# Performance work log

Hardware: AMD Instinct MI355X
Metric: run time of the kernel (lower is better)

## Reference

```python
import jax, jax.numpy as jnp
import numpy as np

N_NODES = 100000


def _gcn_conv(x, W, b, src, dst, ew, num_nodes):
    # PyG GCNConv: symmetric normalization with self-loops already included
    # in (src, dst, ew). deg computed on destination (col) index.
    deg = jax.ops.segment_sum(ew, dst, num_segments=num_nodes)  # [N]
    dinv = jnp.where(deg > 0, jax.lax.rsqrt(deg), 0.0)          # [N]
    norm = dinv[src] * ew * dinv[dst]                           # [E]
    h = x @ W                                                   # [N, out]
    msg = h[src] * norm[:, None]                                # [E, out] gather+scale
    out = jax.ops.segment_sum(msg, dst, num_segments=num_nodes) # scatter-add
    return out + b


def setup_inputs() -> dict:
    key = jax.random.key(0)
    k = jax.random.split(key, 8)
    in_c, hid_c, out_c = 128, 128, 64
    E, EL = 1600000, 200000
    x = jax.random.normal(k[0], (N_NODES, in_c), dtype=jnp.float32)
    edge_index = jax.random.randint(k[1], (2, E), 0, N_NODES, dtype=jnp.int64)
    edge_weight = jax.random.uniform(k[2], (E,), dtype=jnp.float32)
    edge_label_index = jax.random.randint(k[3], (2, EL), 0, N_NODES, dtype=jnp.int64)
    # Glorot-ish params
    W1 = jax.random.normal(k[4], (in_c, hid_c), dtype=jnp.float32) / np.sqrt(in_c)
    b1 = jnp.zeros((hid_c,), dtype=jnp.float32)
    W2 = jax.random.normal(k[5], (hid_c, out_c), dtype=jnp.float32) / np.sqrt(hid_c)
    b2 = jnp.zeros((out_c,), dtype=jnp.float32)
    return {"x": x, "edge_index": edge_index, "edge_weight": edge_weight,
            "edge_label_index": edge_label_index,
            "W1": W1, "b1": b1, "W2": W2, "b2": b2}


def reference(x, edge_index, edge_weight, edge_label_index, W1, b1, W2, b2):
    n = x.shape[0]
    # add self-loops (weight 1.0), static shape
    loop = jnp.arange(n, dtype=edge_index.dtype)
    src = jnp.concatenate([edge_index[0], loop])
    dst = jnp.concatenate([edge_index[1], loop])
    ew = jnp.concatenate([edge_weight, jnp.ones((n,), dtype=edge_weight.dtype)])
    h = jax.nn.relu(_gcn_conv(x, W1, b1, src, dst, ew, n))
    z = _gcn_conv(h, W2, b2, src, dst, ew, n)          # [N, out_c]
    # decode: edge dot-product
    return (z[edge_label_index[0]] * z[edge_label_index[1]]).sum(axis=-1)
```

## Files before the change

kernel.cpp:

```cpp
#include <hip/hip_runtime.h>
#include <math.h>

__global__ __launch_bounds__(256) void gemm128_hist_kernel(
        const float* __restrict__ X, const float* __restrict__ W, float* __restrict__ Y, int n,
        const int* __restrict__ dst, int* __restrict__ cnt, int* __restrict__ rank, int E) {
    constexpr int CG  = 32;
    constexpr int RG  = 8;
    constexpr int M   = 64;
    constexpr int RT  = 8;
    constexpr int KC  = 32;
    constexpr int LDX = 132;
    __shared__ float  Xl[M * LDX];
    __shared__ float4 Wl[KC * CG];

    const int bid = blockIdx.x;
    const int t = threadIdx.x;
    const int EPB = (E + (int)gridDim.x - 1) / (int)gridDim.x;
    const int eBeg = bid * EPB;
    const int eEnd = min(eBeg + EPB, E);

    if ((bid & 1) == 0) {
        for (int e = eBeg + t; e < eEnd; e += 256)
            rank[e] = atomicAdd(&cnt[dst[e]], 1);
    }

    int row0 = bid * M;
    {
        const float4* Xg = (const float4*)X;
        for (int f = t; f < M * 32; f += 256) {
            int r = f >> 5, c4 = f & 31;
            int gr = row0 + r;
            float4 v = make_float4(0.f, 0.f, 0.f, 0.f);
            if (gr < n) v = Xg[(size_t)gr * 32 + c4];
            *(float4*)&Xl[r * LDX + c4 * 4] = v;
        }
    }

    int cg = t % CG;
    int r0 = (t / CG) * RT;

    float4 acc[RT];
#pragma unroll
    for (int r = 0; r < RT; r++) acc[r] = make_float4(0.f, 0.f, 0.f, 0.f);

    const float4* Wg = (const float4*)W;
    for (int kc = 0; kc < 128; kc += KC) {
        __syncthreads();
        for (int f = t; f < KC * CG; f += 256)
            Wl[f] = Wg[(size_t)kc * CG + f];
        __syncthreads();
#pragma unroll 4
        for (int k = 0; k < KC; k += 4) {
            float4 b0 = Wl[(k + 0) * CG + cg];
            float4 b1 = Wl[(k + 1) * CG + cg];
            float4 b2 = Wl[(k + 2) * CG + cg];
            float4 b3 = Wl[(k + 3) * CG + cg];
#pragma unroll
            for (int r = 0; r < RT; r++) {
                float4 a = *(float4*)&Xl[(r0 + r) * LDX + kc + k];
                acc[r].x += a.x * b0.x + a.y * b1.x + a.z * b2.x + a.w * b3.x;
                acc[r].y += a.x * b0.y + a.y * b1.y + a.z * b2.y + a.w * b3.y;
                acc[r].z += a.x * b0.z + a.y * b1.z + a.z * b2.z + a.w * b3.z;
                acc[r].w += a.x * b0.w + a.y * b1.w + a.z * b2.w + a.w * b3.w;
            }
        }
    }

#pragma unroll
    for (int r = 0; r < RT; r++) {
        int gr = row0 + r0 + r;
        if (gr < n) *(float4*)&Y[(size_t)gr * 128 + cg * 4] = acc[r];
    }

    if (bid & 1) {
        for (int e = eBeg + t; e < eEnd; e += 256)
            rank[e] = atomicAdd(&cnt[dst[e]], 1);
    }
}

__global__ __launch_bounds__(256) void scan_block(const int* __restrict__ in, int* __restrict__ out,
                                                  int* __restrict__ bsum, int n) {
    __shared__ int s[256];
    int tid = threadIdx.x;
    int base = blockIdx.x * 1024 + tid * 4;
    int a0 = (base + 0 < n) ? in[base + 0] : 0;
    int a1 = (base + 1 < n) ? in[base + 1] : 0;
    int a2 = (base + 2 < n) ? in[base + 2] : 0;
    int a3 = (base + 3 < n) ? in[base + 3] : 0;
    int tsum = a0 + a1 + a2 + a3;
    s[tid] = tsum;
    __syncthreads();
    for (int off = 1; off < 256; off <<= 1) {
        int v = (tid >= off) ? s[tid - off] : 0;
        __syncthreads();
        s[tid] += v;
        __syncthreads();
    }
    int texcl = s[tid] - tsum;
    if (base + 0 < n) out[base + 0] = texcl;
    if (base + 1 < n) out[base + 1] = texcl + a0;
    if (base + 2 < n) out[base + 2] = texcl + a0 + a1;
    if (base + 3 < n) out[base + 3] = texcl + a0 + a1 + a2;
    if (tid == 255) bsum[blockIdx.x] = s[255];
}

__global__ __launch_bounds__(256) void scan_bsums(int* __restrict__ bsum, int nb) {
    __shared__ int s[256];
    __shared__ int carry_s;
    int tid = threadIdx.x;
    if (tid == 0) carry_s = 0;
    __syncthreads();
    for (int base = 0; base < nb; base += 256) {
        int v = (base + tid < nb) ? bsum[base + tid] : 0;
        int orig = v;
        s[tid] = v;
        __syncthreads();
        for (int off = 1; off < 256; off <<= 1) {
            int u = (tid >= off) ? s[tid - off] : 0;
            __syncthreads();
            s[tid] += u;
            __syncthreads();
        }
        int carry = carry_s;
        int excl = s[tid] - orig + carry;
        if (base + tid < nb) bsum[base + tid] = excl;
        int tot = s[255];
        __syncthreads();
        if (tid == 0) carry_s = carry + tot;
        __syncthreads();
    }
}

__global__ void scan_add(int* __restrict__ rowptr, const int* __restrict__ bscan, int n) {
    int t = blockIdx.x * blockDim.x + threadIdx.x;
    if (t < n) rowptr[t] += bscan[t >> 10];
}

__global__ void scatter_pairs(const int* __restrict__ src, const int* __restrict__ dst,
                              const float* __restrict__ ew, const int* __restrict__ rowptr,
                              const int* __restrict__ rank, int2* __restrict__ pairs, int E) {
    int e = blockIdx.x * blockDim.x + threadIdx.x;
    if (e >= E) return;
    int d = dst[e];
    int p = rowptr[d] + rank[e];
    pairs[p] = make_int2(src[e], __float_as_int(ew[e]));
}

__global__ void deg_dinv_kernel(const int2* __restrict__ pairs, const int* __restrict__ rowptr,
                                float* __restrict__ dinv, int n) {
    int i = blockIdx.x * blockDim.x + threadIdx.x;
    if (i >= n) return;
    int beg = rowptr[i], end = rowptr[i + 1];
    float s = 0.f;
    for (int j = beg; j < end; j++) s += __int_as_float(pairs[j].y);
    dinv[i] = 1.0f / sqrtf(s + 1.0f);
}

__global__ __launch_bounds__(256) void gather_mv_kernel(const float* __restrict__ H,
                                                        const int* __restrict__ rowptr,
                                                        const int2* __restrict__ pairs,
                                                        const float* __restrict__ dinv,
                                                        const float* __restrict__ bias,
                                                        const float* __restrict__ W2,
                                                        float* __restrict__ Z, int n) {
    __shared__ float h1s[8 * 128];
    __shared__ float w2s[128 * 64];
    const int t = threadIdx.x;
    const int nl = t >> 5;
    const int c4 = t & 31;
    const int node = blockIdx.x * 8 + nl;
    const float4* H4 = (const float4*)H;

    {
        const float4* W2g = (const float4*)W2;
        float4* w2s4 = (float4*)w2s;
#pragma unroll
        for (int f = 0; f < 8; f++) w2s4[f * 256 + t] = W2g[f * 256 + t];
    }

    float4 a0 = make_float4(0.f, 0.f, 0.f, 0.f);
    if (node < n) {
        int beg = rowptr[node], end = rowptr[node + 1];
        float di = dinv[node];
        float4 hv = H4[(size_t)node * 32 + c4];
        a0.x = hv.x * di; a0.y = hv.y * di; a0.z = hv.z * di; a0.w = hv.w * di;
        float4 a1 = make_float4(0.f, 0.f, 0.f, 0.f);
        float4 a2 = make_float4(0.f, 0.f, 0.f, 0.f);
        float4 a3 = make_float4(0.f, 0.f, 0.f, 0.f);
        int j = beg;
        for (; j + 8 <= end; j += 8) {
            int2 p0 = pairs[j + 0], p1 = pairs[j + 1], p2 = pairs[j + 2], p3 = pairs[j + 3];
            int2 p4 = pairs[j + 4], p5 = pairs[j + 5], p6 = pairs[j + 6], p7 = pairs[j + 7];
            float4 v0 = H4[(size_t)p0.x * 32 + c4];
            float4 v1 = H4[(size_t)p1.x * 32 + c4];
            float4 v2 = H4[(size_t)p2.x * 32 + c4];
            float4 v3 = H4[(size_t)p3.x * 32 + c4];
            float4 v4 = H4[(size_t)p4.x * 32 + c4];
            float4 v5 = H4[(size_t)p5.x * 32 + c4];
            float4 v6 = H4[(size_t)p6.x * 32 + c4];
            float4 v7 = H4[(size_t)p7.x * 32 + c4];
            float w0 = dinv[p0.x] * __int_as_float(p0.y);
            float w1 = dinv[p1.x] * __int_as_float(p1.y);
            float w2 = dinv[p2.x] * __int_as_float(p2.y);
            float w3 = dinv[p3.x] * __int_as_float(p3.y);
            float w4 = dinv[p4.x] * __int_as_float(p4.y);
            float w5 = dinv[p5.x] * __int_as_float(p5.y);
            float w6 = dinv[p6.x] * __int_as_float(p6.y);
            float w7 = dinv[p7.x] * __int_as_float(p7.y);
            a0.x += v0.x * w0; a0.y += v0.y * w0; a0.z += v0.z * w0; a0.w += v0.w * w0;
            a1.x += v1.x * w1; a1.y += v1.y * w1; a1.z += v1.z * w1; a1.w += v1.w * w1;
            a2.x += v2.x * w2; a2.y += v2.y * w2; a2.z += v2.z * w2; a2.w += v2.w * w2;
            a3.x += v3.x * w3; a3.y += v3.y * w3; a3.z += v3.z * w3; a3.w += v3.w * w3;
            a0.x += v4.x * w4; a0.y += v4.y * w4; a0.z += v4.z * w4; a0.w += v4.w * w4;
            a1.x += v5.x * w5; a1.y += v5.y * w5; a1.z += v5.z * w5; a1.w += v5.w * w5;
            a2.x += v6.x * w6; a2.y += v6.y * w6; a2.z += v6.z * w6; a2.w += v6.w * w6;
            a3.x += v7.x * w7; a3.y += v7.y * w7; a3.z += v7.z * w7; a3.w += v7.w * w7;
        }
        if (j + 4 <= end) {
            int2 p0 = pairs[j + 0], p1 = pairs[j + 1], p2 = pairs[j + 2], p3 = pairs[j + 3];
            float4 v0 = H4[(size_t)p0.x * 32 + c4];
            float4 v1 = H4[(size_t)p1.x * 32 + c4];
            float4 v2 = H4[(size_t)p2.x * 32 + c4];
            float4 v3 = H4[(size_t)p3.x * 32 + c4];
            float w0 = dinv[p0.x] * __int_as_float(p0.y);
            float w1 = dinv[p1.x] * __int_as_float(p1.y);
            float w2 = dinv[p2.x] * __int_as_float(p2.y);
            float w3 = dinv[p3.x] * __int_as_float(p3.y);
            a0.x += v0.x * w0; a0.y += v0.y * w0; a0.z += v0.z * w0; a0.w += v0.w * w0;
            a1.x += v1.x * w1; a1.y += v1.y * w1; a1.z += v1.z * w1; a1.w += v1.w * w1;
            a2.x += v2.x * w2; a2.y += v2.y * w2; a2.z += v2.z * w2; a2.w += v2.w * w2;
            a3.x += v3.x * w3; a3.y += v3.y * w3; a3.z += v3.z * w3; a3.w += v3.w * w3;
            j += 4;
        }
        for (; j < end; j++) {
            int2 pr = pairs[j];
            float w = dinv[pr.x] * __int_as_float(pr.y);
            float4 v = H4[(size_t)pr.x * 32 + c4];
            a0.x += v.x * w; a0.y += v.y * w; a0.z += v.z * w; a0.w += v.w * w;
        }
        float4 bb = ((const float4*)bias)[c4];
        a0.x = fmaxf(((a0.x + a1.x) + (a2.x + a3.x)) * di + bb.x, 0.f);
        a0.y = fmaxf(((a0.y + a1.y) + (a2.y + a3.y)) * di + bb.y, 0.f);
        a0.z = fmaxf(((a0.z + a1.z) + (a2.z + a3.z)) * di + bb.z, 0.f);
        a0.w = fmaxf(((a0.w + a1.w) + (a2.w + a3.w)) * di + bb.w, 0.f);
    }
    *(float4*)&h1s[nl * 128 + c4 * 4] = a0;
    __syncthreads();

    float z0 = 0.f, z1 = 0.f;
    const float* hrow = &h1s[nl * 128];
    const float2* w2c = (const float2*)w2s;
#pragma unroll 8
    for (int k = 0; k < 128; k++) {
        float hk = hrow[k];
        float2 w = w2c[k * 32 + c4];
        z0 += hk * w.x;
        z1 += hk * w.y;
    }
    if (node < n) *(float2*)&Z[(size_t)node * 64 + c4 * 2] = make_float2(z0, z1);
}

template<int C, bool RELU>
__global__ __launch_bounds__(256) void gather_reduce(const float* __restrict__ H,
                                                     const int* __restrict__ rowptr,
                                                     const int2* __restrict__ pairs,
                                                     const float* __restrict__ dinv,
                                                     const float* __restrict__ bias,
                                                     float* __restrict__ out, int n) {
    constexpr int TPN = C / 4;
    int t = blockIdx.x * blockDim.x + threadIdx.x;
    int node = t / TPN;
    int c4 = t % TPN;
    if (node >= n) return;
    const float4* H4 = (const float4*)H;
    int beg = rowptr[node], end = rowptr[node + 1];
    float di = dinv[node];
    float4 hv = H4[(size_t)node * TPN + c4];
    float4 bb = ((const float4*)bias)[c4];
    float4 a0, a1, a2, a3;
    a0.x = hv.x * di; a0.y = hv.y * di; a0.z = hv.z * di; a0.w = hv.w * di;
    a1 = make_float4(0.f, 0.f, 0.f, 0.f);
    a2 = make_float4(0.f, 0.f, 0.f, 0.f);
    a3 = make_float4(0.f, 0.f, 0.f, 0.f);
    int j = beg;
    for (; j + 8 <= end; j += 8) {
        int2 p0 = pairs[j + 0], p1 = pairs[j + 1], p2 = pairs[j + 2], p3 = pairs[j + 3];
        int2 p4 = pairs[j + 4], p5 = pairs[j + 5], p6 = pairs[j + 6], p7 = pairs[j + 7];
        float4 v0 = H4[(size_t)p0.x * TPN + c4];
        float4 v1 = H4[(size_t)p1.x * TPN + c4];
        float4 v2 = H4[(size_t)p2.x * TPN + c4];
        float4 v3 = H4[(size_t)p3.x * TPN + c4];
        float4 v4 = H4[(size_t)p4.x * TPN + c4];
        float4 v5 = H4[(size_t)p5.x * TPN + c4];
        float4 v6 = H4[(size_t)p6.x * TPN + c4];
        float4 v7 = H4[(size_t)p7.x * TPN + c4];
        float w0 = dinv[p0.x] * __int_as_float(p0.y);
        float w1 = dinv[p1.x] * __int_as_float(p1.y);
        float w2 = dinv[p2.x] * __int_as_float(p2.y);
        float w3 = dinv[p3.x] * __int_as_float(p3.y);
        float w4 = dinv[p4.x] * __int_as_float(p4.y);
        float w5 = dinv[p5.x] * __int_as_float(p5.y);
        float w6 = dinv[p6.x] * __int_as_float(p6.y);
        float w7 = dinv[p7.x] * __int_as_float(p7.y);
        a0.x += v0.x * w0; a0.y += v0.y * w0; a0.z += v0.z * w0; a0.w += v0.w * w0;
        a1.x += v1.x * w1; a1.y += v1.y * w1; a1.z += v1.z * w1; a1.w += v1.w * w1;
        a2.x += v2.x * w2; a2.y += v2.y * w2; a2.z += v2.z * w2; a2.w += v2.w * w2;
        a3.x += v3.x * w3; a3.y += v3.y * w3; a3.z += v3.z * w3; a3.w += v3.w * w3;
        a0.x += v4.x * w4; a0.y += v4.y * w4; a0.z += v4.z * w4; a0.w += v4.w * w4;
        a1.x += v5.x * w5; a1.y += v5.y * w5; a1.z += v5.z * w5; a1.w += v5.w * w5;
        a2.x += v6.x * w6; a2.y += v6.y * w6; a2.z += v6.z * w6; a2.w += v6.w * w6;
        a3.x += v7.x * w7; a3.y += v7.y * w7; a3.z += v7.z * w7; a3.w += v7.w * w7;
    }
    if (j + 4 <= end) {
        int2 p0 = pairs[j + 0], p1 = pairs[j + 1], p2 = pairs[j + 2], p3 = pairs[j + 3];
        float4 v0 = H4[(size_t)p0.x * TPN + c4];
        float4 v1 = H4[(size_t)p1.x * TPN + c4];
        float4 v2 = H4[(size_t)p2.x * TPN + c4];
        float4 v3 = H4[(size_t)p3.x * TPN + c4];
        float w0 = dinv[p0.x] * __int_as_float(p0.y);
        float w1 = dinv[p1.x] * __int_as_float(p1.y);
        float w2 = dinv[p2.x] * __int_as_float(p2.y);
        float w3 = dinv[p3.x] * __int_as_float(p3.y);
        a0.x += v0.x * w0; a0.y += v0.y * w0; a0.z += v0.z * w0; a0.w += v0.w * w0;
        a1.x += v1.x * w1; a1.y += v1.y * w1; a1.z += v1.z * w1; a1.w += v1.w * w1;
        a2.x += v2.x * w2; a2.y += v2.y * w2; a2.z += v2.z * w2; a2.w += v2.w * w2;
        a3.x += v3.x * w3; a3.y += v3.y * w3; a3.z += v3.z * w3; a3.w += v3.w * w3;
        j += 4;
    }
    for (; j < end; j++) {
        int2 pr = pairs[j];
        float w = dinv[pr.x] * __int_as_float(pr.y);
        float4 v = H4[(size_t)pr.x * TPN + c4];
        a0.x += v.x * w; a0.y += v.y * w; a0.z += v.z * w; a0.w += v.w * w;
    }
    float4 acc;
    acc.x = ((a0.x + a1.x) + (a2.x + a3.x)) * di + bb.x;
    acc.y = ((a0.y + a1.y) + (a2.y + a3.y)) * di + bb.y;
    acc.z = ((a0.z + a1.z) + (a2.z + a3.z)) * di + bb.z;
    acc.w = ((a0.w + a1.w) + (a2.w + a3.w)) * di + bb.w;
    if (RELU) {
        acc.x = fmaxf(acc.x, 0.f);
        acc.y = fmaxf(acc.y, 0.f);
        acc.z = fmaxf(acc.z, 0.f);
        acc.w = fmaxf(acc.w, 0.f);
    }
    *(float4*)&out[(size_t)node * C + c4 * 4] = acc;
}

__global__ void decode_kernel(const float* __restrict__ Z, const int* __restrict__ ea,
                              const int* __restrict__ eb, float* __restrict__ out, int L) {
    int t = blockIdx.x * blockDim.x + threadIdx.x;
    int e = t >> 4;
    int c = (t & 15) << 2;
    if (e >= L) return;
    float4 za = *(const float4*)&Z[(size_t)ea[e] * 64 + c];
    float4 zb = *(const float4*)&Z[(size_t)eb[e] * 64 + c];
    float p = za.x * zb.x + za.y * zb.y + za.z * zb.z + za.w * zb.w;
    p += __shfl_xor(p, 1);
    p += __shfl_xor(p, 2);
    p += __shfl_xor(p, 4);
    p += __shfl_xor(p, 8);
    if ((t & 15) == 0) out[e] = p;
}

extern "C" void kernel_launch(void* const* d_in, const int* in_sizes, int n_in,
                              void* d_out, int out_size, void* d_ws, size_t ws_size,
                              hipStream_t stream) {
    const float* x   = (const float*)d_in[0];
    const int*   ei  = (const int*)d_in[1];
    const float* ew  = (const float*)d_in[2];
    const int*   eli = (const int*)d_in[3];
    const float* W1  = (const float*)d_in[4];
    const float* b1  = (const float*)d_in[5];
    const float* W2  = (const float*)d_in[6];
    const float* b2  = (const float*)d_in[7];
    float* out = (float*)d_out;

    const int N = in_sizes[0] / 128;
    const int E = in_sizes[2];
    const int L = in_sizes[3] / 2;
    const int NP = ((N + 255) / 256) * 256;

    float* ws     = (float*)d_ws;
    float* dinv   = ws;
    int*   cnt    = (int*)(ws + NP);
    int*   rowptr = cnt + NP;
    int*   bsum   = rowptr + NP;
    int*   rank   = bsum + 1024;
    int2*  pairs  = (int2*)(rank + E);
    float* A      = (float*)(pairs + E);
    float* B      = A + (size_t)NP * 128;

    const int n1 = N + 1;
    const int nb = (n1 + 1023) / 1024;

    hipMemsetAsync(cnt, 0, (size_t)n1 * 4, stream);

    const int Gg = (N + 63) / 64;
    gemm128_hist_kernel<<<Gg, 256, 0, stream>>>(x, W1, A, N, ei + E, cnt, rank, E);

    scan_block<<<nb, 256, 0, stream>>>(cnt, rowptr, bsum, n1);
    scan_bsums<<<1, 256, 0, stream>>>(bsum, nb);
    scan_add<<<(n1 + 255) / 256, 256, 0, stream>>>(rowptr, bsum, n1);
    scatter_pairs<<<(E + 255) / 256, 256, 0, stream>>>(ei, ei + E, ew, rowptr, rank, pairs, E);
    deg_dinv_kernel<<<(N + 255) / 256, 256, 0, stream>>>(pairs, rowptr, dinv, N);

    gather_mv_kernel<<<(N + 7) / 8, 256, 0, stream>>>(A, rowptr, pairs, dinv, b1, W2, B, N);

    gather_reduce<64, false><<<(N * 16 + 255) / 256, 256, 0, stream>>>(B, rowptr, pairs, dinv, b2, A, N);

    decode_kernel<<<(L * 16 + 255) / 256, 256, 0, stream>>>(A, eli, eli + L, out, L);
}
```

Baseline: 488.2 us.

## Prefold source-node normalization into edge weights and enlarge gather_mv blocks

A new premul kernel multiplies each CSR edge weight by dinv of its source node once. Both aggregation passes then read the folded weight and skip the random dinv[src] gather per edge. gather_mv_kernel also moves to 512 threads covering 16 nodes per block, so the shared W2 load is spread over more nodes. The cost is an extra read-modify-write pass over 1.6M pairs and a kernel launch, plus the register and LDS pressure that comes with 512-thread blocks and launch_bounds(512,8).

```diff
diff --git a/kernel.cpp b/kernel.cpp
--- a/kernel.cpp
+++ b/kernel.cpp
@@ -156,26 +156,34 @@
     dinv[i] = 1.0f / sqrtf(s + 1.0f);
 }
 
-__global__ __launch_bounds__(256) void gather_mv_kernel(const float* __restrict__ H,
-                                                        const int* __restrict__ rowptr,
-                                                        const int2* __restrict__ pairs,
-                                                        const float* __restrict__ dinv,
-                                                        const float* __restrict__ bias,
-                                                        const float* __restrict__ W2,
-                                                        float* __restrict__ Z, int n) {
-    __shared__ float h1s[8 * 128];
+__global__ void premul_kernel(int2* __restrict__ pairs, const float* __restrict__ dinv, int E) {
+    int e = blockIdx.x * blockDim.x + threadIdx.x;
+    if (e >= E) return;
+    int2 p = pairs[e];
+    p.y = __float_as_int(__int_as_float(p.y) * dinv[p.x]);
+    pairs[e] = p;
+}
+
+__global__ __launch_bounds__(512, 8) void gather_mv_kernel(const float* __restrict__ H,
+                                                           const int* __restrict__ rowptr,
+                                                           const int2* __restrict__ pairs,
+                                                           const float* __restrict__ dinv,
+                                                           const float* __restrict__ bias,
+                                                           const float* __restrict__ W2,
+                                                           float* __restrict__ Z, int n) {
+    __shared__ float h1s[16 * 128];
     __shared__ float w2s[128 * 64];
     const int t = threadIdx.x;
     const int nl = t >> 5;
     const int c4 = t & 31;
-    const int node = blockIdx.x * 8 + nl;
+    const int node = blockIdx.x * 16 + nl;
     const float4* H4 = (const float4*)H;
 
     {
         const float4* W2g = (const float4*)W2;
         float4* w2s4 = (float4*)w2s;
 #pragma unroll
-        for (int f = 0; f < 8; f++) w2s4[f * 256 + t] = W2g[f * 256 + t];
+        for (int f = 0; f < 4; f++) w2s4[f * 512 + t] = W2g[f * 512 + t];
     }
 
     float4 a0 = make_float4(0.f, 0.f, 0.f, 0.f);
@@ -199,14 +207,14 @@
             float4 v5 = H4[(size_t)p5.x * 32 + c4];
             float4 v6 = H4[(size_t)p6.x * 32 + c4];
             float4 v7 = H4[(size_t)p7.x * 32 + c4];
-            float w0 = dinv[p0.x] * __int_as_float(p0.y);
-            float w1 = dinv[p1.x] * __int_as_float(p1.y);
-            float w2 = dinv[p2.x] * __int_as_float(p2.y);
-            float w3 = dinv[p3.x] * __int_as_float(p3.y);
-            float w4 = dinv[p4.x] * __int_as_float(p4.y);
-            float w5 = dinv[p5.x] * __int_as_float(p5.y);
-            float w6 = dinv[p6.x] * __int_as_float(p6.y);
-            float w7 = dinv[p7.x] * __int_as_float(p7.y);
+            float w0 = __int_as_float(p0.y);
+            float w1 = __int_as_float(p1.y);
+            float w2 = __int_as_float(p2.y);
+            float w3 = __int_as_float(p3.y);
+            float w4 = __int_as_float(p4.y);
+            float w5 = __int_as_float(p5.y);
+            float w6 = __int_as_float(p6.y);
+            float w7 = __int_as_float(p7.y);
             a0.x += v0.x * w0; a0.y += v0.y * w0; a0.z += v0.z * w0; a0.w += v0.w * w0;
             a1.x += v1.x * w1; a1.y += v1.y * w1; a1.z += v1.z * w1; a1.w += v1.w * w1;
             a2.x += v2.x * w2; a2.y += v2.y * w2; a2.z += v2.z * w2; a2.w += v2.w * w2;
@@ -222,10 +230,10 @@
             float4 v1 = H4[(size_t)p1.x * 32 + c4];
             float4 v2 = H4[(size_t)p2.x * 32 + c4];
             float4 v3 = H4[(size_t)p3.x * 32 + c4];
-            float w0 = dinv[p0.x] * __int_as_float(p0.y);
-            float w1 = dinv[p1.x] * __int_as_float(p1.y);
-            float w2 = dinv[p2.x] * __int_as_float(p2.y);
-            float w3 = dinv[p3.x] * __int_as_float(p3.y);
+            float w0 = __int_as_float(p0.y);
+            float w1 = __int_as_float(p1.y);
+            float w2 = __int_as_float(p2.y);
+            float w3 = __int_as_float(p3.y);
             a0.x += v0.x * w0; a0.y += v0.y * w0; a0.z += v0.z * w0; a0.w += v0.w * w0;
             a1.x += v1.x * w1; a1.y += v1.y * w1; a1.z += v1.z * w1; a1.w += v1.w * w1;
             a2.x += v2.x * w2; a2.y += v2.y * w2; a2.z += v2.z * w2; a2.w += v2.w * w2;
@@ -234,7 +242,7 @@
         }
         for (; j < end; j++) {
             int2 pr = pairs[j];
-            float w = dinv[pr.x] * __int_as_float(pr.y);
+            float w = __int_as_float(pr.y);
             float4 v = H4[(size_t)pr.x * 32 + c4];
             a0.x += v.x * w; a0.y += v.y * w; a0.z += v.z * w; a0.w += v.w * w;
         }
@@ -294,14 +302,14 @@
         float4 v5 = H4[(size_t)p5.x * TPN + c4];
         float4 v6 = H4[(size_t)p6.x * TPN + c4];
         float4 v7 = H4[(size_t)p7.x * TPN + c4];
-        float w0 = dinv[p0.x] * __int_as_float(p0.y);
-        float w1 = dinv[p1.x] * __int_as_float(p1.y);
-        float w2 = dinv[p2.x] * __int_as_float(p2.y);
-        float w3 = dinv[p3.x] * __int_as_float(p3.y);
-        float w4 = dinv[p4.x] * __int_as_float(p4.y);
-        float w5 = dinv[p5.x] * __int_as_float(p5.y);
-        float w6 = dinv[p6.x] * __int_as_float(p6.y);
-        float w7 = dinv[p7.x] * __int_as_float(p7.y);
+        float w0 = __int_as_float(p0.y);
+        float w1 = __int_as_float(p1.y);
+        float w2 = __int_as_float(p2.y);
+        float w3 = __int_as_float(p3.y);
+        float w4 = __int_as_float(p4.y);
+        float w5 = __int_as_float(p5.y);
+        float w6 = __int_as_float(p6.y);
+        float w7 = __int_as_float(p7.y);
         a0.x += v0.x * w0; a0.y += v0.y * w0; a0.z += v0.z * w0; a0.w += v0.w * w0;
         a1.x += v1.x * w1; a1.y += v1.y * w1; a1.z += v1.z * w1; a1.w += v1.w * w1;
         a2.x += v2.x * w2; a2.y += v2.y * w2; a2.z += v2.z * w2; a2.w += v2.w * w2;
@@ -317,10 +325,10 @@
         float4 v1 = H4[(size_t)p1.x * TPN + c4];
         float4 v2 = H4[(size_t)p2.x * TPN + c4];
         float4 v3 = H4[(size_t)p3.x * TPN + c4];
-        float w0 = dinv[p0.x] * __int_as_float(p0.y);
-        float w1 = dinv[p1.x] * __int_as_float(p1.y);
-        float w2 = dinv[p2.x] * __int_as_float(p2.y);
-        float w3 = dinv[p3.x] * __int_as_float(p3.y);
+        float w0 = __int_as_float(p0.y);
+        float w1 = __int_as_float(p1.y);
+        float w2 = __int_as_float(p2.y);
+        float w3 = __int_as_float(p3.y);
         a0.x += v0.x * w0; a0.y += v0.y * w0; a0.z += v0.z * w0; a0.w += v0.w * w0;
         a1.x += v1.x * w1; a1.y += v1.y * w1; a1.z += v1.z * w1; a1.w += v1.w * w1;
         a2.x += v2.x * w2; a2.y += v2.y * w2; a2.z += v2.z * w2; a2.w += v2.w * w2;
@@ -329,7 +337,7 @@
     }
     for (; j < end; j++) {
         int2 pr = pairs[j];
-        float w = dinv[pr.x] * __int_as_float(pr.y);
+        float w = __int_as_float(pr.y);
         float4 v = H4[(size_t)pr.x * TPN + c4];
         a0.x += v.x * w; a0.y += v.y * w; a0.z += v.z * w; a0.w += v.w * w;
     }
@@ -404,8 +412,9 @@
     scan_add<<<(n1 + 255) / 256, 256, 0, stream>>>(rowptr, bsum, n1);
     scatter_pairs<<<(E + 255) / 256, 256, 0, stream>>>(ei, ei + E, ew, rowptr, rank, pairs, E);
     deg_dinv_kernel<<<(N + 255) / 256, 256, 0, stream>>>(pairs, rowptr, dinv, N);
-
-    gather_mv_kernel<<<(N + 7) / 8, 256, 0, stream>>>(A, rowptr, pairs, dinv, b1, W2, B, N);
+    premul_kernel<<<(E + 255) / 256, 256, 0, stream>>>(pairs, dinv, E);
+
+    gather_mv_kernel<<<(N + 15) / 16, 512, 0, stream>>>(A, rowptr, pairs, dinv, b1, W2, B, N);
 
     gather_reduce<64, false><<<(N * 16 + 255) / 256, 256, 0, stream>>>(B, rowptr, pairs, dinv, b2, A, N);
 
```

New measurement: 499.9 us. 1.02x slower.
